# Optimization experiments

Measured on AMD Instinct MI355X. Metric: run time of the kernel, lower is better.

## Reference

```python
import jax, jax.numpy as jnp
import numpy as np

ROUTING_ITERS = 3
EPS = 1e-12


def squash(s):
    # squash over both pose-matrix dims (axis=[-2,-1])
    n2 = jnp.sum(s * s, axis=(-2, -1), keepdims=True)
    n = jnp.sqrt(n2 + EPS)
    return s * (n2 / (1.0 + n2)) / n


def setup_inputs() -> dict:
    key = jax.random.key(0)
    k1, k2, k3 = jax.random.split(key, 3)
    B, I, O = 32, 4096, 32
    input_poses = jax.random.normal(k1, (B, I, 4, 4), dtype=jnp.float32)
    input_activations = jax.random.uniform(k2, (B, I), dtype=jnp.float32)
    # weight: [num_capsules, num_input_caps, 4, 4] (trans_in=trans_out=False for 4x4->4x4)
    w = jax.random.normal(k3, (O, I, 4, 4), dtype=jnp.float32) * 0.05
    return {"input_poses": input_poses, "input_activations": input_activations, "w": w}


def reference(input_poses, input_activations, w):
    # votes: expand_dims(poses,1) @ w, broadcast over output capsules -> [B,O,I,4,4]
    votes = jnp.einsum("bixy,oiyz->boixz", input_poses, w)
    B, O, I = votes.shape[0], votes.shape[1], votes.shape[2]

    # dynamic routing (routing-by-agreement)
    b = jnp.zeros((B, O, I), dtype=votes.dtype)
    s = None
    for it in range(ROUTING_ITERS):
        c = jax.nn.softmax(b, axis=1)  # couple over output capsules
        s = jnp.einsum("boi,boixy->boxy", c, votes)  # weighted sum [B,O,4,4]
        if it < ROUTING_ITERS - 1:
            v = squash(s)
            b = b + jnp.einsum("boixy,boxy->boi", votes, v)

    capsule_poses = squash(s)  # activation == 'squash'
    capsule_activations = jnp.sqrt(jnp.sum(capsule_poses * capsule_poses, axis=(-2, -1)) + EPS)
    return capsule_poses, capsule_activations
```

## Files before the change

### kernel.cpp

```cpp
#include <hip/hip_runtime.h>
#include <math.h>


#define NB 32
#define NI 4096
#define NO 32
#define I_TILE 16
#define NCHUNK (NI / I_TILE)
#define B_TILE 8
#define NBG (NB / B_TILE)
#define SOFF (NB * NO * 16)
#define EPSF 1e-12f

#define W_OSTR 10
#define W_ISTR (32 * W_OSTR)
#define W_WORDS (I_TILE * W_ISTR)
#define P_WORDS (B_TILE * I_TILE * 8)

typedef _Float16 v2h __attribute__((ext_vector_type(2)));

#if __has_builtin(__builtin_amdgcn_fdot2)
__device__ __forceinline__ float fdot2(v2h a, v2h b, float c) {
    return __builtin_amdgcn_fdot2(a, b, c, false);
}
#else
__device__ __forceinline__ float fdot2(v2h a, v2h b, float c) {
    return fmaf((float)a.x, (float)b.x, fmaf((float)a.y, (float)b.y, c));
}
#endif

#if __has_builtin(__builtin_amdgcn_cvt_pkrtz)
__device__ __forceinline__ v2h pk2h(float a, float b) {
    return __builtin_bit_cast(v2h, __builtin_amdgcn_cvt_pkrtz(a, b));
}
#else
__device__ __forceinline__ v2h pk2h(float a, float b) {
    v2h r; r.x = (_Float16)a; r.y = (_Float16)b; return r;
}
#endif

__device__ __forceinline__ v2h bch(unsigned u) {
    return __builtin_bit_cast(v2h, u);
}

__device__ __forceinline__ float dot4(const float4 a, const float4 b) {
    return fmaf(a.x, b.x, fmaf(a.y, b.y, fmaf(a.z, b.z, a.w * b.w)));
}

__device__ __forceinline__ void fma4(float4& s, const float c, const float4 t) {
    s.x = fmaf(c, t.x, s.x);
    s.y = fmaf(c, t.y, s.y);
    s.z = fmaf(c, t.z, s.z);
    s.w = fmaf(c, t.w, s.w);
}

template <int CTRL>
__device__ __forceinline__ float dpp_add(float x) {
    int xi = __builtin_bit_cast(int, x);
    int yi = __builtin_amdgcn_update_dpp(0, xi, CTRL, 0xf, 0xf, false);
    return x + __builtin_bit_cast(float, yi);
}

__device__ __forceinline__ float sum32(float x) {
    x = dpp_add<0xB1>(x);
    x = dpp_add<0x4E>(x);
    x = dpp_add<0x141>(x);
    x = dpp_add<0x140>(x);
#if __has_builtin(__builtin_amdgcn_permlane16_swap)
    typedef unsigned uv2 __attribute__((ext_vector_type(2)));
    const unsigned xi = __builtin_bit_cast(unsigned, x);
    uv2 r = __builtin_amdgcn_permlane16_swap(xi, xi, false, false);
    return __builtin_bit_cast(float, r.x) + __builtin_bit_cast(float, r.y);
#else
    int t = __builtin_amdgcn_ds_swizzle(__builtin_bit_cast(int, x), 0x401F);
    return x + __builtin_bit_cast(float, t);
#endif
}

__global__ __launch_bounds__(256, 4) void caps_pass_h(
    const float* __restrict__ poses, const float* __restrict__ w,
    const float* __restrict__ v_buf, float* __restrict__ s_part,
    const int pass)
{
    __shared__ unsigned wsw[W_WORDS];
    __shared__ unsigned psw[P_WORDS];
    const int tid    = threadIdx.x;
    const int chunk  = blockIdx.x;
    const int bgroup = blockIdx.y;
    const int ibase  = chunk * I_TILE;

    #pragma unroll
    for (int r = 0; r < 4; ++r) {
        const int idx = r * 256 + tid;
        const int o_l = idx >> 5;
        const int l   = idx & 31;
        const int i_l = l >> 1;
        const int m   = l & 1;
        const float* g = w + (((size_t)o_l * NI + ibase + i_l) << 4) + (m << 3);
        const float4 A = *(const float4*)g;
        const float4 B = *(const float4*)(g + 4);
        const v2h c0 = pk2h(A.x, B.x), c1 = pk2h(A.y, B.y);
        const v2h c2 = pk2h(A.z, B.z), c3 = pk2h(A.w, B.w);
        const int base = i_l * W_ISTR + o_l * W_OSTR + (m << 2);
        *(uint2*)&wsw[base]     = make_uint2(__builtin_bit_cast(unsigned, c0),
                                             __builtin_bit_cast(unsigned, c1));
        *(uint2*)&wsw[base + 2] = make_uint2(__builtin_bit_cast(unsigned, c2),
                                             __builtin_bit_cast(unsigned, c3));
    }
    #pragma unroll
    for (int r = 0; r < 2; ++r) {
        const int idx = r * 256 + tid;
        const int b_l = idx >> 6;
        const int l   = idx & 63;
        const int i_l = l >> 2;
        const int x   = l & 3;
        const float4 row = *(const float4*)(
            poses + (((size_t)(bgroup * B_TILE + b_l) * NI + ibase + i_l) << 4)
                  + (x << 2));
        const v2h c0 = pk2h(row.x, row.y), c1 = pk2h(row.z, row.w);
        *(uint2*)&psw[((b_l * I_TILE + i_l) << 3) + (x << 1)] =
            make_uint2(__builtin_bit_cast(unsigned, c0),
                       __builtin_bit_cast(unsigned, c1));
    }

    const int o    = tid & 31;
    const int bsub = tid >> 5;
    const int b    = bgroup * B_TILE + bsub;
    const int bo   = b * NO + o;

    float4 vv0 = {0,0,0,0}, vv1 = {0,0,0,0}, vv2 = {0,0,0,0}, vv3 = {0,0,0,0};
    if (pass > 0) {
        const float4* vp = (const float4*)(v_buf + (bo << 4));
        vv0 = vp[0]; vv1 = vp[1]; vv2 = vp[2]; vv3 = vp[3];
    }

    const unsigned* wrow = &wsw[o * W_OSTR];
    const unsigned* prow = &psw[(bsub * I_TILE) << 3];

    __syncthreads();

    float4 s0 = {0,0,0,0}, s1 = {0,0,0,0}, s2 = {0,0,0,0}, s3 = {0,0,0,0};

    #pragma unroll 2
    for (int i = 0; i < I_TILE; ++i) {
        const uint2 wa = *(const uint2*)&wrow[i * W_ISTR + 0];
        const uint2 wb = *(const uint2*)&wrow[i * W_ISTR + 2];
        const uint2 wc = *(const uint2*)&wrow[i * W_ISTR + 4];
        const uint2 wd = *(const uint2*)&wrow[i * W_ISTR + 6];
        const uint4 pa = *(const uint4*)&prow[(i << 3) + 0];
        const uint4 pb = *(const uint4*)&prow[(i << 3) + 4];

        const v2h p00 = bch(pa.x), p01 = bch(pa.y);
        const v2h p10 = bch(pa.z), p11 = bch(pa.w);
        const v2h p20 = bch(pb.x), p21 = bch(pb.y);
        const v2h p30 = bch(pb.z), p31 = bch(pb.w);
        const v2h w00 = bch(wa.x), w01 = bch(wa.y);
        const v2h w02 = bch(wb.x), w03 = bch(wb.y);
        const v2h w10 = bch(wc.x), w11 = bch(wc.y);
        const v2h w12 = bch(wd.x), w13 = bch(wd.y);

        float4 t0, t1, t2, t3;
        t0.x = fdot2(p00, w00, fdot2(p01, w10, 0.0f));
        t0.y = fdot2(p00, w01, fdot2(p01, w11, 0.0f));
        t0.z = fdot2(p00, w02, fdot2(p01, w12, 0.0f));
        t0.w = fdot2(p00, w03, fdot2(p01, w13, 0.0f));
        t1.x = fdot2(p10, w00, fdot2(p11, w10, 0.0f));
        t1.y = fdot2(p10, w01, fdot2(p11, w11, 0.0f));
        t1.z = fdot2(p10, w02, fdot2(p11, w12, 0.0f));
        t1.w = fdot2(p10, w03, fdot2(p11, w13, 0.0f));
        t2.x = fdot2(p20, w00, fdot2(p21, w10, 0.0f));
        t2.y = fdot2(p20, w01, fdot2(p21, w11, 0.0f));
        t2.z = fdot2(p20, w02, fdot2(p21, w12, 0.0f));
        t2.w = fdot2(p20, w03, fdot2(p21, w13, 0.0f));
        t3.x = fdot2(p30, w00, fdot2(p31, w10, 0.0f));
        t3.y = fdot2(p30, w01, fdot2(p31, w11, 0.0f));
        t3.z = fdot2(p30, w02, fdot2(p31, w12, 0.0f));
        t3.w = fdot2(p30, w03, fdot2(p31, w13, 0.0f));

        float cc;
        if (pass == 0) {
            cc = 1.0f / 32.0f;
        } else {
            const float d = dot4(t0,vv0) + dot4(t1,vv1)
                          + dot4(t2,vv2) + dot4(t3,vv3);
            const float e  = __expf(d);
            const float es = sum32(e);
            cc = __fdividef(e, es);
        }
        fma4(s0, cc, t0); fma4(s1, cc, t1);
        fma4(s2, cc, t2); fma4(s3, cc, t3);
    }

    float4* sp = (float4*)(s_part + ((size_t)chunk * (NB * NO) + bo) * 16);
    sp[0] = s0; sp[1] = s1; sp[2] = s2; sp[3] = s3;
}

__global__ __launch_bounds__(256) void caps_reduce(
    const float* __restrict__ s_part, float* __restrict__ v_buf,
    float* __restrict__ out, const int pass)
{
    const int e  = threadIdx.x & 63;
    const int c4 = threadIdx.x >> 6;
    const int eg = blockIdx.x * 64 + e;

    float acc = 0.0f;
    #pragma unroll 8
    for (int j = 0; j < NCHUNK / 4; ++j) {
        const int c = c4 * (NCHUNK / 4) + j;
        acc += s_part[(size_t)c * SOFF + eg];
    }
    __shared__ float red[4][64];
    red[c4][e] = acc;
    __syncthreads();

    if (threadIdx.x < 64) {
        const float a = red[0][e] + red[1][e] + red[2][e] + red[3][e];
        float x = a * a;
        #pragma unroll
        for (int msk = 8; msk >= 1; msk >>= 1)
            x += __shfl_xor(x, msk, 16);
        const float n2 = x;
        const float n  = sqrtf(n2 + EPSF);
        const float sc = (n2 / (1.0f + n2)) / n;
        if (pass < 2) {
            const float vold = (pass == 0) ? 0.0f : v_buf[eg];
            v_buf[eg] = fmaf(sc, a, vold);
        } else {
            out[eg] = sc * a;
            if ((e & 15) == 0)
                out[NB * NO * 16 + (eg >> 4)] = sqrtf(n2 * sc * sc + EPSF);
        }
    }
}

#define FB_CHUNKS 32
#define FB_IPB (NI / FB_CHUNKS)

__device__ __forceinline__ float4 row_mm(const float4 p, const float4 w0,
                                         const float4 w1, const float4 w2,
                                         const float4 w3) {
    float4 r;
    r.x = fmaf(p.x, w0.x, fmaf(p.y, w1.x, fmaf(p.z, w2.x, p.w * w3.x)));
    r.y = fmaf(p.x, w0.y, fmaf(p.y, w1.y, fmaf(p.z, w2.y, p.w * w3.y)));
    r.z = fmaf(p.x, w0.z, fmaf(p.y, w1.z, fmaf(p.z, w2.z, p.w * w3.z)));
    r.w = fmaf(p.x, w0.w, fmaf(p.y, w1.w, fmaf(p.z, w2.w, p.w * w3.w)));
    return r;
}

__global__ __launch_bounds__(256) void caps_pass_fb(
    const float* __restrict__ poses, const float* __restrict__ w,
    const float* __restrict__ v_buf, float* __restrict__ s_buf, const int mode)
{
    const int tid   = threadIdx.x;
    const int b     = blockIdx.y;
    const int chunk = blockIdx.x;
    const int o     = tid & 31;
    const int g     = tid >> 5;

    float4 v0 = {0,0,0,0}, v1 = {0,0,0,0}, v2 = {0,0,0,0}, v3 = {0,0,0,0};
    if (mode != 0) {
        const float4* vp = (const float4*)(v_buf + (((b * NO) + o) << 4));
        v0 = vp[0]; v1 = vp[1]; v2 = vp[2]; v3 = vp[3];
    }
    float4 s0 = {0,0,0,0}, s1 = {0,0,0,0}, s2 = {0,0,0,0}, s3 = {0,0,0,0};
    const int ibase = chunk * FB_IPB + g;
    #pragma unroll 4
    for (int it = 0; it < FB_IPB / 8; ++it) {
        const int i = ibase + (it << 3);
        const float4* ppf = (const float4*)(poses + ((((size_t)b * NI) + i) << 4));
        const float4 p0 = ppf[0], p1 = ppf[1], p2 = ppf[2], p3 = ppf[3];
        const float4* wpf = (const float4*)(w + ((((size_t)o * NI) + i) << 4));
        const float4 w0 = wpf[0], w1 = wpf[1], w2 = wpf[2], w3 = wpf[3];
        const float4 t0 = row_mm(p0, w0, w1, w2, w3);
        const float4 t1 = row_mm(p1, w0, w1, w2, w3);
        const float4 t2 = row_mm(p2, w0, w1, w2, w3);
        const float4 t3 = row_mm(p3, w0, w1, w2, w3);
        float cc;
        if (mode == 0) {
            cc = 1.0f / 32.0f;
        } else {
            float d = dot4(t0,v0) + dot4(t1,v1) + dot4(t2,v2) + dot4(t3,v3);
            const float e  = __expf(d);
            const float es = sum32(e);
            cc = __fdividef(e, es);
        }
        fma4(s0, cc, t0); fma4(s1, cc, t1);
        fma4(s2, cc, t2); fma4(s3, cc, t3);
    }
    __shared__ float red[8][32][16];
    float4* rp = (float4*)&red[g][o][0];
    rp[0] = s0; rp[1] = s1; rp[2] = s2; rp[3] = s3;
    __syncthreads();
    for (int idx = tid; idx < NO * 16; idx += 256) {
        const int oo = idx >> 4;
        const int k  = idx & 15;
        float acc = red[0][oo][k];
        #pragma unroll
        for (int gg = 1; gg < 8; ++gg) acc += red[gg][oo][k];
        atomicAdd(&s_buf[(((b * NO) + oo) << 4) + k], acc);
    }
}

__global__ __launch_bounds__(256) void caps_squash_fb(
    float* __restrict__ s_buf, float* __restrict__ v_buf,
    float* __restrict__ out, const int mode)
{
    const int idx = blockIdx.x * 256 + threadIdx.x;
    if (idx >= NB * NO) return;
    float4* sp = (float4*)(s_buf + (idx << 4));
    const float4 s0 = sp[0], s1 = sp[1], s2 = sp[2], s3 = sp[3];
    const float n2 = dot4(s0,s0) + dot4(s1,s1) + dot4(s2,s2) + dot4(s3,s3);
    const float n  = sqrtf(n2 + EPSF);
    const float sc = (n2 / (1.0f + n2)) / n;
    if (mode == 2) {
        float4* op = (float4*)(out + (idx << 4));
        op[0] = make_float4(sc*s0.x, sc*s0.y, sc*s0.z, sc*s0.w);
        op[1] = make_float4(sc*s1.x, sc*s1.y, sc*s1.z, sc*s1.w);
        op[2] = make_float4(sc*s2.x, sc*s2.y, sc*s2.z, sc*s2.w);
        op[3] = make_float4(sc*s3.x, sc*s3.y, sc*s3.z, sc*s3.w);
        out[NB * NO * 16 + idx] = sqrtf(n2 * sc * sc + EPSF);
    } else {
        float4* vp = (float4*)(v_buf + (idx << 4));
        float4 a0 = {0,0,0,0}, a1 = {0,0,0,0}, a2 = {0,0,0,0}, a3 = {0,0,0,0};
        if (mode != 0) { a0 = vp[0]; a1 = vp[1]; a2 = vp[2]; a3 = vp[3]; }
        vp[0] = make_float4(fmaf(sc,s0.x,a0.x), fmaf(sc,s0.y,a0.y), fmaf(sc,s0.z,a0.z), fmaf(sc,s0.w,a0.w));
        vp[1] = make_float4(fmaf(sc,s1.x,a1.x), fmaf(sc,s1.y,a1.y), fmaf(sc,s1.z,a1.z), fmaf(sc,s1.w,a1.w));
        vp[2] = make_float4(fmaf(sc,s2.x,a2.x), fmaf(sc,s2.y,a2.y), fmaf(sc,s2.z,a2.z), fmaf(sc,s2.w,a2.w));
        vp[3] = make_float4(fmaf(sc,s3.x,a3.x), fmaf(sc,s3.y,a3.y), fmaf(sc,s3.z,a3.z), fmaf(sc,s3.w,a3.w));
        const float4 z = {0,0,0,0};
        sp[0] = z; sp[1] = z; sp[2] = z; sp[3] = z;
    }
}

extern "C" void kernel_launch(void* const* d_in, const int* in_sizes, int n_in,
                              void* d_out, int out_size, void* d_ws, size_t ws_size,
                              hipStream_t stream) {
    const float* poses = (const float*)d_in[0];
    const float* w     = (const float*)d_in[2];
    float* out = (float*)d_out;

    const size_t need = ((size_t)NCHUNK * SOFF + SOFF) * sizeof(float);
    if (ws_size >= need) {
        float* s_part = (float*)d_ws;
        float* v_buf  = s_part + (size_t)NCHUNK * SOFF;
        dim3 gp(NCHUNK, NBG), blk(256), gr(256);
        for (int pass = 0; pass < 3; ++pass) {
            caps_pass_h<<<gp, blk, 0, stream>>>(poses, w, v_buf, s_part, pass);
            caps_reduce<<<gr, blk, 0, stream>>>(s_part, v_buf, out, pass);
        }
    } else {
        float* s_buf = (float*)d_ws;
        float* v_buf = s_buf + SOFF;
        (void)hipMemsetAsync(s_buf, 0, SOFF * sizeof(float), stream);
        dim3 grid(FB_CHUNKS, NB), block(256);
        for (int pass = 0; pass < 3; ++pass) {
            caps_pass_fb<<<grid, block, 0, stream>>>(poses, w, v_buf, s_buf, pass);
            caps_squash_fb<<<4, 256, 0, stream>>>(s_buf, v_buf, out, pass);
        }
    }
}
```

Measured before the change: 131.0 us.

## Fuse all routing passes into one cooperative kernel with grid syncs

Replaces the six-launch sequence (three pass kernels plus three reduce kernels) with a single cooperative kernel. Weights and poses are staged into shared memory once, the routing logits' agreement vector is carried in registers across passes, and partial sums are reduced after grid-wide barriers. This removes repeated launch overhead and the re-staging of W and poses per pass. The cost is three grid syncs and the need for all 1024 blocks to be co-resident. If the cooperative launch fails, the code falls back to the old multi-kernel path.

Measured after the change: 130.5 us. No clear change (-0.4%).

```diff
diff --git a/kernel.cpp b/kernel.cpp
--- a/kernel.cpp
+++ b/kernel.cpp
@@ -1,4 +1,5 @@
 #include <hip/hip_runtime.h>
+#include <hip/hip_cooperative_groups.h>
 #include <math.h>
 
 
@@ -17,6 +18,8 @@
 #define W_WORDS (I_TILE * W_ISTR)
 #define P_WORDS (B_TILE * I_TILE * 8)
 
+namespace cg = cooperative_groups;
+
 typedef _Float16 v2h __attribute__((ext_vector_type(2)));
 
 #if __has_builtin(__builtin_amdgcn_fdot2)
@@ -52,6 +55,10 @@
     s.y = fmaf(c, t.y, s.y);
     s.z = fmaf(c, t.z, s.z);
     s.w = fmaf(c, t.w, s.w);
+}
+
+__device__ __forceinline__ void add4(float4& s, const float4 t) {
+    s.x += t.x; s.y += t.y; s.z += t.z; s.w += t.w;
 }
 
 template <int CTRL>
@@ -75,6 +82,171 @@
     int t = __builtin_amdgcn_ds_swizzle(__builtin_bit_cast(int, x), 0x401F);
     return x + __builtin_bit_cast(float, t);
 #endif
+}
+
+__global__ __launch_bounds__(256, 4) void caps_fused(
+    const float* __restrict__ poses, const float* __restrict__ w,
+    float* __restrict__ s_part, float* __restrict__ v_contrib,
+    float* __restrict__ out)
+{
+    __shared__ unsigned wsw[W_WORDS];
+    __shared__ unsigned psw[P_WORDS];
+    __shared__ float red[16][17];
+
+    const int tid    = threadIdx.x;
+    const int chunk  = blockIdx.x;
+    const int bgroup = blockIdx.y;
+    const int ibase  = chunk * I_TILE;
+
+    #pragma unroll
+    for (int r = 0; r < 4; ++r) {
+        const int idx = r * 256 + tid;
+        const int o_l = idx >> 5;
+        const int l   = idx & 31;
+        const int i_l = l >> 1;
+        const int m   = l & 1;
+        const float* g = w + (((size_t)o_l * NI + ibase + i_l) << 4) + (m << 3);
+        const float4 A = *(const float4*)g;
+        const float4 B = *(const float4*)(g + 4);
+        const v2h c0 = pk2h(A.x, B.x), c1 = pk2h(A.y, B.y);
+        const v2h c2 = pk2h(A.z, B.z), c3 = pk2h(A.w, B.w);
+        const int base = i_l * W_ISTR + o_l * W_OSTR + (m << 2);
+        *(uint2*)&wsw[base]     = make_uint2(__builtin_bit_cast(unsigned, c0),
+                                             __builtin_bit_cast(unsigned, c1));
+        *(uint2*)&wsw[base + 2] = make_uint2(__builtin_bit_cast(unsigned, c2),
+                                             __builtin_bit_cast(unsigned, c3));
+    }
+    #pragma unroll
+    for (int r = 0; r < 2; ++r) {
+        const int idx = r * 256 + tid;
+        const int b_l = idx >> 6;
+        const int l   = idx & 63;
+        const int i_l = l >> 2;
+        const int x   = l & 3;
+        const float4 row = *(const float4*)(
+            poses + (((size_t)(bgroup * B_TILE + b_l) * NI + ibase + i_l) << 4)
+                  + (x << 2));
+        const v2h c0 = pk2h(row.x, row.y), c1 = pk2h(row.z, row.w);
+        *(uint2*)&psw[((b_l * I_TILE + i_l) << 3) + (x << 1)] =
+            make_uint2(__builtin_bit_cast(unsigned, c0),
+                       __builtin_bit_cast(unsigned, c1));
+    }
+
+    const int o    = tid & 31;
+    const int bsub = tid >> 5;
+    const int b    = bgroup * B_TILE + bsub;
+    const int bo   = b * NO + o;
+    const int rbo  = bgroup * NCHUNK + chunk;
+
+    const unsigned* wrow = &wsw[o * W_OSTR];
+    const unsigned* prow = &psw[(bsub * I_TILE) << 3];
+
+    float4 vv0 = {0,0,0,0}, vv1 = {0,0,0,0}, vv2 = {0,0,0,0}, vv3 = {0,0,0,0};
+
+    cg::grid_group gg = cg::this_grid();
+
+    __syncthreads();
+
+    for (int pass = 0; pass < 3; ++pass) {
+        float4 s0 = {0,0,0,0}, s1 = {0,0,0,0}, s2 = {0,0,0,0}, s3 = {0,0,0,0};
+
+        #pragma unroll 2
+        for (int i = 0; i < I_TILE; ++i) {
+            const uint2 wa = *(const uint2*)&wrow[i * W_ISTR + 0];
+            const uint2 wb = *(const uint2*)&wrow[i * W_ISTR + 2];
+            const uint2 wc = *(const uint2*)&wrow[i * W_ISTR + 4];
+            const uint2 wd = *(const uint2*)&wrow[i * W_ISTR + 6];
+            const uint4 pa = *(const uint4*)&prow[(i << 3) + 0];
+            const uint4 pb = *(const uint4*)&prow[(i << 3) + 4];
+
+            const v2h p00 = bch(pa.x), p01 = bch(pa.y);
+            const v2h p10 = bch(pa.z), p11 = bch(pa.w);
+            const v2h p20 = bch(pb.x), p21 = bch(pb.y);
+            const v2h p30 = bch(pb.z), p31 = bch(pb.w);
+            const v2h w00 = bch(wa.x), w01 = bch(wa.y);
+            const v2h w02 = bch(wb.x), w03 = bch(wb.y);
+            const v2h w10 = bch(wc.x), w11 = bch(wc.y);
+            const v2h w12 = bch(wd.x), w13 = bch(wd.y);
+
+            float4 t0, t1, t2, t3;
+            t0.x = fdot2(p00, w00, fdot2(p01, w10, 0.0f));
+            t0.y = fdot2(p00, w01, fdot2(p01, w11, 0.0f));
+            t0.z = fdot2(p00, w02, fdot2(p01, w12, 0.0f));
+            t0.w = fdot2(p00, w03, fdot2(p01, w13, 0.0f));
+            t1.x = fdot2(p10, w00, fdot2(p11, w10, 0.0f));
+            t1.y = fdot2(p10, w01, fdot2(p11, w11, 0.0f));
+            t1.z = fdot2(p10, w02, fdot2(p11, w12, 0.0f));
+            t1.w = fdot2(p10, w03, fdot2(p11, w13, 0.0f));
+            t2.x = fdot2(p20, w00, fdot2(p21, w10, 0.0f));
+            t2.y = fdot2(p20, w01, fdot2(p21, w11, 0.0f));
+            t2.z = fdot2(p20, w02, fdot2(p21, w12, 0.0f));
+            t2.w = fdot2(p20, w03, fdot2(p21, w13, 0.0f));
+            t3.x = fdot2(p30, w00, fdot2(p31, w10, 0.0f));
+            t3.y = fdot2(p30, w01, fdot2(p31, w11, 0.0f));
+            t3.z = fdot2(p30, w02, fdot2(p31, w12, 0.0f));
+            t3.w = fdot2(p30, w03, fdot2(p31, w13, 0.0f));
+
+            float cc;
+            if (pass == 0) {
+                cc = 1.0f / 32.0f;
+            } else {
+                const float d = dot4(t0,vv0) + dot4(t1,vv1)
+                              + dot4(t2,vv2) + dot4(t3,vv3);
+                const float e  = __expf(d);
+                const float es = sum32(e);
+                cc = __fdividef(e, es);
+            }
+            fma4(s0, cc, t0); fma4(s1, cc, t1);
+            fma4(s2, cc, t2); fma4(s3, cc, t3);
+        }
+
+        float4* sp = (float4*)(s_part + (((size_t)bo * NCHUNK + chunk) << 4));
+        sp[0] = s0; sp[1] = s1; sp[2] = s2; sp[3] = s3;
+
+        __threadfence();
+        gg.sync();
+        __threadfence();
+
+        {
+            const int k   = tid & 15;
+            const int grp = tid >> 4;
+            const float* base = s_part + ((size_t)rbo << 12);
+            float acc = 0.0f;
+            #pragma unroll
+            for (int j = 0; j < 16; ++j)
+                acc += base[((grp + (j << 4)) << 4) + k];
+            red[grp][k] = acc;
+        }
+        __syncthreads();
+        if (tid < 16) {
+            float a = red[0][tid];
+            #pragma unroll
+            for (int g2 = 1; g2 < 16; ++g2) a += red[g2][tid];
+            float x = a * a;
+            #pragma unroll
+            for (int msk = 8; msk >= 1; msk >>= 1)
+                x += __shfl_xor(x, msk, 16);
+            const float n2 = x;
+            const float n  = sqrtf(n2 + EPSF);
+            const float sc = (n2 / (1.0f + n2)) / n;
+            if (pass < 2) {
+                v_contrib[(rbo << 4) + tid] = sc * a;
+            } else {
+                out[(rbo << 4) + tid] = sc * a;
+                if (tid == 0)
+                    out[NB * NO * 16 + rbo] = sqrtf(n2 * sc * sc + EPSF);
+            }
+        }
+        if (pass == 2) break;
+
+        __threadfence();
+        gg.sync();
+        __threadfence();
+
+        const float4* vp = (const float4*)(v_contrib + (bo << 4));
+        add4(vv0, vp[0]); add4(vv1, vp[1]);
+        add4(vv2, vp[2]); add4(vv3, vp[3]);
+    }
 }
 
 __global__ __launch_bounds__(256, 4) void caps_pass_h(
@@ -335,6 +507,7 @@
 extern "C" void kernel_launch(void* const* d_in, const int* in_sizes, int n_in,
                               void* d_out, int out_size, void* d_ws, size_t ws_size,
                               hipStream_t stream) {
+    (void)in_sizes; (void)n_in; (void)out_size;
     const float* poses = (const float*)d_in[0];
     const float* w     = (const float*)d_in[2];
     float* out = (float*)d_out;
@@ -343,6 +516,18 @@
     if (ws_size >= need) {
         float* s_part = (float*)d_ws;
         float* v_buf  = s_part + (size_t)NCHUNK * SOFF;
+
+        static int coop_state = -1;
+        if (coop_state != 0) {
+            void* args[] = { (void*)&poses, (void*)&w, (void*)&s_part,
+                             (void*)&v_buf, (void*)&out };
+            hipError_t e = hipLaunchCooperativeKernel(
+                caps_fused, dim3(NCHUNK, NBG), dim3(256), args, 0u, stream);
+            if (e == hipSuccess) { coop_state = 1; return; }
+            coop_state = 0;
+            (void)hipGetLastError();
+        }
+
         dim3 gp(NCHUNK, NBG), blk(256), gr(256);
         for (int pass = 0; pass < 3; ++pass) {
             caps_pass_h<<<gp, blk, 0, stream>>>(poses, w, v_buf, s_part, pass);
```
